# Optimization experiments

Hardware: AMD Instinct MI355X
Metric: run time of the kernel (lower is better)

The kernel has to match this reference:

```python
import jax, jax.numpy as jnp
import numpy as np

EPS = 1e-12

def _l2n(x):
    return x / jnp.sqrt(jnp.maximum(jnp.sum(x * x, axis=-1, keepdims=True), EPS))

def _sn_kernel(w, u):
    # One power iteration of spectral normalization (TF SpectralNormalization._compute_weights).
    wr = w.reshape(-1, w.shape[-1])           # [in, out] (1x1 conv kernel flattened)
    v = _l2n(u @ wr.T)                        # [1, in]
    u2 = _l2n(v @ wr)                         # [1, out]
    u2 = jax.lax.stop_gradient(u2)
    v = jax.lax.stop_gradient(v)
    sigma = (v @ wr) @ u2.T                   # [1, 1]
    return w / sigma[0, 0]

def setup_inputs() -> dict:
    key = jax.random.key(0)
    ks = jax.random.split(key, 14)
    B, H, W, C = 8, 64, 64, 256
    d = C // 8
    inp = {
        'x':  jax.random.normal(ks[0], (B, H, W, C), jnp.float32),
        'wf': jax.random.normal(ks[1], (C, d), jnp.float32) * 0.02,
        'bf': jax.random.normal(ks[2], (d,), jnp.float32) * 0.02,
        'uf': jax.random.normal(ks[3], (1, d), jnp.float32) * 0.02,
        'wg': jax.random.normal(ks[4], (C, d), jnp.float32) * 0.02,
        'bg': jax.random.normal(ks[5], (d,), jnp.float32) * 0.02,
        'ug': jax.random.normal(ks[6], (1, d), jnp.float32) * 0.02,
        'wh': jax.random.normal(ks[7], (C, d), jnp.float32) * 0.02,
        'bh': jax.random.normal(ks[8], (d,), jnp.float32) * 0.02,
        'uh': jax.random.normal(ks[9], (1, d), jnp.float32) * 0.02,
        'wv': jax.random.normal(ks[10], (d, C), jnp.float32) * 0.02,
        'bv': jax.random.normal(ks[11], (C,), jnp.float32) * 0.02,
        'uv': jax.random.normal(ks[12], (1, C), jnp.float32) * 0.02,
        'gamma': jax.random.normal(ks[13], (1,), jnp.float32) * 0.1,
    }
    return inp

def reference(x, wf, bf, uf, wg, bg, ug, wh, bh, uh, wv, bv, uv, gamma):
    B, H, W, C = x.shape
    N = H * W
    # spectrally-normalized 1x1 conv kernels
    kf = _sn_kernel(wf, uf)
    kg = _sn_kernel(wg, ug)
    kh = _sn_kernel(wh, uh)
    kv = _sn_kernel(wv, uv)
    # 1x1 convs == channel matmuls on flattened spatial dims
    xf = x.reshape(B, N, C)
    f = xf @ kf + bf            # [B, N, d]
    g = xf @ kg + bg            # [B, N, d]
    h = xf @ kh + bh            # [B, N, d]
    s = jnp.einsum('bnd,bmd->bnm', g, f)   # [B, N, N]
    beta = jax.nn.softmax(s, axis=-1)
    v = jnp.einsum('bnm,bmd->bnd', beta, h)  # [B, N, d]
    o = v @ kv + bv             # [B, N, C]
    out = gamma[0] * o.reshape(B, H, W, C) + x
    return out
```

## Files before the change

### kernel.cpp

```cpp
#include <hip/hip_runtime.h>
#include <math.h>

typedef __attribute__((ext_vector_type(8))) short bf16x8;
typedef __attribute__((ext_vector_type(4))) short bf16x4;
typedef __attribute__((ext_vector_type(4))) float f32x4;

#define LOG2E 1.4426950408889634f

#if __has_builtin(__builtin_amdgcn_exp2f)
#define EXP2(x) __builtin_amdgcn_exp2f(x)
#else
#define EXP2(x) exp2f(x)
#endif

static __device__ __forceinline__ short f2bf(float f) {
  unsigned u = __builtin_bit_cast(unsigned, f);
  u = u + 0x7FFFu + ((u >> 16) & 1u);
  return (short)(u >> 16);
}

struct SigArgs {
  const float* w[4];
  const float* u[4];
  int din[4];
  int dout[4];
};

__global__ __launch_bounds__(256) void sigma_kernel(SigArgs a, float* scales) {
  int b = blockIdx.x;
  const float* w = a.w[b];
  const float* u = a.u[b];
  int IN = a.din[b], OUT = a.dout[b];
  __shared__ float sv[256];
  __shared__ float red[256];
  int tid = threadIdx.x;

  float t = 0.f;
  if (tid < IN) {
    for (int j = 0; j < OUT; j++) t += u[j] * w[tid * OUT + j];
  }
  red[tid] = t * t;
  __syncthreads();
  for (int st = 128; st > 0; st >>= 1) {
    if (tid < st) red[tid] += red[tid + st];
    __syncthreads();
  }
  float nv = sqrtf(fmaxf(red[0], 1e-12f));
  sv[tid] = (tid < IN) ? t / nv : 0.f;
  __syncthreads();

  float s2 = 0.f;
  if (tid < OUT) {
    float sum = 0.f;
    for (int i = 0; i < IN; i++) sum += sv[i] * w[i * OUT + tid];
    s2 = sum * sum;
  }
  red[tid] = s2;
  __syncthreads();
  for (int st = 128; st > 0; st >>= 1) {
    if (tid < st) red[tid] += red[tid + st];
    __syncthreads();
  }
  if (tid == 0) {
    float sum2 = red[0];
    float sigma = sum2 / sqrtf(fmaxf(sum2, 1e-12f));
    scales[b] = 1.0f / sigma;
  }
}

__global__ __launch_bounds__(256) void prep_weights(
    const float* __restrict__ wf, const float* __restrict__ wg,
    const float* __restrict__ wh, const float* __restrict__ wv,
    const float* __restrict__ scales, short* __restrict__ Wt,
    short* __restrict__ Kvt) {
  int idx = blockIdx.x * 256 + threadIdx.x;
  if (idx < 96 * 256) {
    int c = idx >> 8, k = idx & 255;
    int sel = c >> 5, cc = c & 31;
    const float* w = (sel == 0) ? wf : ((sel == 1) ? wg : wh);
    float sc = scales[sel] * ((sel == 1) ? LOG2E : 1.0f);
    Wt[idx] = f2bf(w[k * 32 + cc] * sc);
  } else {
    int i2 = idx - 96 * 256;
    if (i2 < 256 * 32) {
      int c = i2 >> 5, k = i2 & 31;
      Kvt[i2] = f2bf(wv[k * 256 + c] * scales[3]);
    }
  }
}

__global__ __launch_bounds__(256) void proj_kernel(
    const float* __restrict__ x, const short* __restrict__ Wt,
    const float* __restrict__ bf_, const float* __restrict__ bg_,
    const float* __restrict__ bh_, short* __restrict__ fo,
    short* __restrict__ go, short* __restrict__ hto) {
  __shared__ __align__(16) short xs[64][264];
  __shared__ float hsh[64][33];
  int row0 = blockIdx.x * 64;
  int tid = threadIdx.x;
  int wave = tid >> 6;
  int lane = tid & 63;
  int quad = lane >> 4, l16 = lane & 15;
  int rbase = row0 + wave * 16;

  const float4* xb = (const float4*)(x + (size_t)row0 * 256);
#pragma unroll
  for (int i = 0; i < 16; i++) {
    int e4 = i * 256 + tid;
    float4 v = xb[e4];
    int e = e4 * 4;
    int r = e >> 8, c = e & 255;
    bf16x4 s4;
    s4[0] = f2bf(v.x); s4[1] = f2bf(v.y); s4[2] = f2bf(v.z); s4[3] = f2bf(v.w);
    *(bf16x4*)&xs[r][c] = s4;
  }
  __syncthreads();

  f32x4 acc[6];
#pragma unroll
  for (int t = 0; t < 6; t++) acc[t] = (f32x4){0.f, 0.f, 0.f, 0.f};

#pragma unroll
  for (int kc = 0; kc < 256; kc += 32) {
    bf16x8 af = *(const bf16x8*)&xs[wave * 16 + l16][kc + quad * 8];
#pragma unroll
    for (int t = 0; t < 6; t++) {
      bf16x8 bfr = *(const bf16x8*)(Wt + (t * 16 + l16) * 256 + kc + quad * 8);
      acc[t] = __builtin_amdgcn_mfma_f32_16x16x32_bf16(af, bfr, acc[t], 0, 0, 0);
    }
  }

  int b = row0 >> 12;
  int n0 = row0 & 4095;
#pragma unroll
  for (int t = 0; t < 4; t++) {
    int c = t * 16 + l16;
    int sel = c >> 5, cc = c & 31;
    float bb = sel ? (bg_[cc] * LOG2E) : bf_[cc];
    short* dst = sel ? go : fo;
#pragma unroll
    for (int r = 0; r < 4; r++) {
      int row = rbase + quad * 4 + r;
      dst[(size_t)row * 32 + cc] = f2bf(acc[t][r] + bb);
    }
  }
#pragma unroll
  for (int t = 4; t < 6; t++) {
    int cc = (t - 4) * 16 + l16;
    float bb = bh_[cc];
#pragma unroll
    for (int r = 0; r < 4; r++) {
      hsh[wave * 16 + quad * 4 + r][cc] = acc[t][r] + bb;
    }
  }
  __syncthreads();
  {
    int d = threadIdx.x >> 3, ng = threadIdx.x & 7;
    bf16x8 tmp;
#pragma unroll
    for (int i = 0; i < 8; i++) tmp[i] = f2bf(hsh[ng * 8 + i][d]);
    *(bf16x8*)(hto + (size_t)(b * 32 + d) * 4096 + n0 + ng * 8) = tmp;
  }
}

__global__ __launch_bounds__(256) void attn_kernel(
    const short* __restrict__ g_, const short* __restrict__ f_,
    const short* __restrict__ ht_, short* __restrict__ po,
    float* __restrict__ ls) {
  __shared__ __align__(16) short psh[4][4][16][72];
  int b = blockIdx.y;
  int z = blockIdx.z;
  int wave = threadIdx.x >> 6;
  int lane = threadIdx.x & 63;
  int quad = lane >> 4, l16 = lane & 15;
  int qbase = blockIdx.x * 256 + wave * 64;
  int kc0 = z * 1024;

  const short* fb = f_ + (size_t)b * 4096 * 32;
  const short* hb = ht_ + (size_t)b * 32 * 4096;

  bf16x8 ga[4];
#pragma unroll
  for (int grp = 0; grp < 4; grp++)
    ga[grp] = *(const bf16x8*)(g_ + (size_t)(b * 4096 + qbase + grp * 16 + l16) * 32 +
                               quad * 8);

  f32x4 oacc[4][2];
#pragma unroll
  for (int grp = 0; grp < 4; grp++)
#pragma unroll
    for (int dt = 0; dt < 2; dt++) oacc[grp][dt] = (f32x4){0.f, 0.f, 0.f, 0.f};
  float lsum[4] = {0.f, 0.f, 0.f, 0.f};

  bf16x8 fA[4], fB[4];
#pragma unroll
  for (int t = 0; t < 4; t++)
    fA[t] = *(const bf16x8*)(fb + (size_t)(kc0 + t * 16 + l16) * 32 + quad * 8);

  auto chunk = [&](int kc, bf16x8* FC, bf16x8* FN) {
    bf16x8 hfr[2][2];
#pragma unroll
    for (int half = 0; half < 2; half++)
#pragma unroll
      for (int dt = 0; dt < 2; dt++)
        hfr[half][dt] = *(const bf16x8*)(hb + (size_t)(dt * 16 + l16) * 4096 +
                                         kc + half * 32 + quad * 8);
    int kn = (kc + 64 < kc0 + 1024) ? kc + 64 : kc0;
#pragma unroll
    for (int t = 0; t < 4; t++)
      FN[t] = *(const bf16x8*)(fb + (size_t)(kn + t * 16 + l16) * 32 + quad * 8);

#pragma unroll
    for (int grp = 0; grp < 4; grp++) {
      f32x4 s[4];
#pragma unroll
      for (int t = 0; t < 4; t++)
        s[t] = __builtin_amdgcn_mfma_f32_16x16x32_bf16(
            FC[t], ga[grp], (f32x4){0.f, 0.f, 0.f, 0.f}, 0, 0, 0);

      unsigned long long pk[4];
#pragma unroll
      for (int t = 0; t < 4; t++) {
        float p0 = EXP2(s[t][0]);
        float p1 = EXP2(s[t][1]);
        float p2 = EXP2(s[t][2]);
        float p3 = EXP2(s[t][3]);
        lsum[grp] += (p0 + p1) + (p2 + p3);
        unsigned lo = __builtin_amdgcn_perm(__builtin_bit_cast(unsigned, p1),
                                            __builtin_bit_cast(unsigned, p0),
                                            0x07060302u);
        unsigned hi = __builtin_amdgcn_perm(__builtin_bit_cast(unsigned, p3),
                                            __builtin_bit_cast(unsigned, p2),
                                            0x07060302u);
        pk[t] = ((unsigned long long)hi << 32) | lo;
      }

      unsigned long long* prow64 = (unsigned long long*)&psh[wave][grp][l16][0];
      asm volatile("" ::: "memory");
#pragma unroll
      for (int t = 0; t < 4; t++) prow64[4 * t + quad] = pk[t];
      asm volatile("" ::: "memory");

#pragma unroll
      for (int half = 0; half < 2; half++) {
        bf16x8 pa = *(const bf16x8*)(&psh[wave][grp][l16][half * 32 + quad * 8]);
#pragma unroll
        for (int dt = 0; dt < 2; dt++)
          oacc[grp][dt] = __builtin_amdgcn_mfma_f32_16x16x32_bf16(
              hfr[half][dt], pa, oacc[grp][dt], 0, 0, 0);
      }
    }
  };

  for (int it = 0; it < 16; it += 2) {
    chunk(kc0 + it * 64, fA, fB);
    chunk(kc0 + it * 64 + 64, fB, fA);
  }

#pragma unroll
  for (int grp = 0; grp < 4; grp++) {
    lsum[grp] += __shfl_xor(lsum[grp], 16);
    lsum[grp] += __shfl_xor(lsum[grp], 32);
  }

#pragma unroll
  for (int grp = 0; grp < 4; grp++) {
    size_t row = (size_t)b * 4096 + qbase + grp * 16 + l16;
    short* pod = po + ((size_t)z * 32768 + row) * 32;
#pragma unroll
    for (int dt = 0; dt < 2; dt++) {
      unsigned w0 = (unsigned)(unsigned short)f2bf(oacc[grp][dt][0]) |
                    ((unsigned)(unsigned short)f2bf(oacc[grp][dt][1]) << 16);
      unsigned w1 = (unsigned)(unsigned short)f2bf(oacc[grp][dt][2]) |
                    ((unsigned)(unsigned short)f2bf(oacc[grp][dt][3]) << 16);
      unsigned* dst = (unsigned*)(pod + dt * 16 + quad * 4);
      dst[0] = w0;
      dst[1] = w1;
    }
  }
  if (lane < 16) {
#pragma unroll
    for (int grp = 0; grp < 4; grp++)
      ls[(size_t)z * 32768 + (size_t)b * 4096 + qbase + grp * 16 + lane] = lsum[grp];
  }
}

__global__ __launch_bounds__(256) void outproj_kernel(
    const short* __restrict__ po, const float* __restrict__ ls,
    const short* __restrict__ Kvt, const float* __restrict__ bv,
    const float* __restrict__ gamma, const float* __restrict__ x,
    float* __restrict__ out) {
  __shared__ __align__(16) float osh[4][16][260];
  int row0 = blockIdx.x * 64;
  int wave = threadIdx.x >> 6, lane = threadIdx.x & 63;
  int quad = lane >> 4, l16 = lane & 15;
  int rbase = row0 + wave * 16;
  size_t row = (size_t)rbase + l16;

  float vacc[8];
#pragma unroll
  for (int j = 0; j < 8; j++) vacc[j] = 0.f;
#pragma unroll
  for (int z = 0; z < 4; z++) {
    const unsigned* p =
        (const unsigned*)(po + ((size_t)z * 32768 + row) * 32 + quad * 8);
#pragma unroll
    for (int j = 0; j < 4; j++) {
      unsigned w = p[j];
      vacc[2 * j] += __builtin_bit_cast(float, w << 16);
      vacc[2 * j + 1] += __builtin_bit_cast(float, w & 0xFFFF0000u);
    }
  }
  float l = ls[row] + ls[32768 + row] + ls[65536 + row] + ls[98304 + row];
  float inv = 1.0f / l;
  bf16x8 va;
#pragma unroll
  for (int j = 0; j < 8; j++) va[j] = f2bf(vacc[j] * inv);

  float gm = gamma[0];

  f32x4 acc[16];
#pragma unroll
  for (int t = 0; t < 16; t++) {
    bf16x8 kf = *(const bf16x8*)(Kvt + (t * 16 + l16) * 32 + quad * 8);
    acc[t] = __builtin_amdgcn_mfma_f32_16x16x32_bf16(
        va, kf, (f32x4){0.f, 0.f, 0.f, 0.f}, 0, 0, 0);
  }
#pragma unroll
  for (int t = 0; t < 16; t++) {
    float bb = bv[t * 16 + l16];
#pragma unroll
    for (int r = 0; r < 4; r++) {
      osh[wave][quad * 4 + r][t * 16 + l16] = acc[t][r] + bb;
    }
  }
  asm volatile("" ::: "memory");
  {
    int r_l = lane >> 2, c_l = lane & 3;
    int orow = row0 + wave * 16 + r_l;
    const float* oshr = &osh[wave][r_l][0];
    const float4* xr = (const float4*)(x + (size_t)orow * 256);
    float4* outr = (float4*)(out + (size_t)orow * 256);
#pragma unroll
    for (int i = 0; i < 16; i++) {
      int c4 = c_l + i * 4;
      float4 o4 = *(const float4*)&oshr[c4 * 4];
      float4 xv = xr[c4];
      float4 ov;
      ov.x = gm * o4.x + xv.x;
      ov.y = gm * o4.y + xv.y;
      ov.z = gm * o4.z + xv.z;
      ov.w = gm * o4.w + xv.w;
      outr[c4] = ov;
    }
  }
}

extern "C" void kernel_launch(void* const* d_in, const int* in_sizes, int n_in,
                              void* d_out, int out_size, void* d_ws,
                              size_t ws_size, hipStream_t stream) {
  const float* x = (const float*)d_in[0];
  const float* wf = (const float*)d_in[1];
  const float* bf = (const float*)d_in[2];
  const float* uf = (const float*)d_in[3];
  const float* wg = (const float*)d_in[4];
  const float* bg = (const float*)d_in[5];
  const float* ug = (const float*)d_in[6];
  const float* wh = (const float*)d_in[7];
  const float* bh = (const float*)d_in[8];
  const float* uh = (const float*)d_in[9];
  const float* wv = (const float*)d_in[10];
  const float* bv = (const float*)d_in[11];
  const float* uv = (const float*)d_in[12];
  const float* gamma = (const float*)d_in[13];
  float* out = (float*)d_out;

  char* ws = (char*)d_ws;
  float* scales = (float*)ws;
  short* Wt = (short*)(ws + 1024);
  short* Kvt = (short*)(ws + 64 * 1024);
  short* fo = (short*)(ws + 2u * 1024 * 1024);
  short* go = (short*)(ws + 4u * 1024 * 1024);
  short* hto = (short*)(ws + 6u * 1024 * 1024);
  short* po = (short*)(ws + 10u * 1024 * 1024);
  float* lsp = (float*)(ws + 18u * 1024 * 1024);

  SigArgs sa;
  sa.w[0] = wf; sa.u[0] = uf; sa.din[0] = 256; sa.dout[0] = 32;
  sa.w[1] = wg; sa.u[1] = ug; sa.din[1] = 256; sa.dout[1] = 32;
  sa.w[2] = wh; sa.u[2] = uh; sa.din[2] = 256; sa.dout[2] = 32;
  sa.w[3] = wv; sa.u[3] = uv; sa.din[3] = 32;  sa.dout[3] = 256;

  sigma_kernel<<<4, 256, 0, stream>>>(sa, scales);
  prep_weights<<<128, 256, 0, stream>>>(wf, wg, wh, wv, scales, Wt, Kvt);
  proj_kernel<<<512, 256, 0, stream>>>(x, Wt, bf, bg, bh, fo, go, hto);
  attn_kernel<<<dim3(16, 8, 4), 256, 0, stream>>>(go, fo, hto, po, lsp);
  outproj_kernel<<<512, 256, 0, stream>>>(po, lsp, Kvt, bv, gamma, x, out);
}
```

Before: 184.7 us.

## Software-pipeline PV MFMA one group behind the QK exp stage

Restructures the attention inner loop so each group's P·V MFMAs run one step behind its score/exp stage, reading the previous group's P tile from LDS before the current group's P is written. The P store and reload for the same group are no longer back to back, which gives the LDS write latency time to resolve and lets MFMA work overlap with exp work. This needs double-buffered H fragments across chunks, a zero-initialized prologue (zeroed P slot 3 and H buffer) and an epilogue that drains the last group. The cost is extra registers for the second H buffer, which may reduce occupancy.

```diff
diff --git a/kernel.cpp b/kernel.cpp
--- a/kernel.cpp
+++ b/kernel.cpp
@@ -192,31 +192,42 @@
     for (int dt = 0; dt < 2; dt++) oacc[grp][dt] = (f32x4){0.f, 0.f, 0.f, 0.f};
   float lsum[4] = {0.f, 0.f, 0.f, 0.f};
 
+  {
+    unsigned long long* p3 = (unsigned long long*)&psh[wave][3][l16][0];
+#pragma unroll
+    for (int t = 0; t < 4; t++) p3[4 * t + quad] = 0ull;
+  }
+  bf16x8 hA[2][2], hB[2][2];
+#pragma unroll
+  for (int half = 0; half < 2; half++)
+#pragma unroll
+    for (int dt = 0; dt < 2; dt++) hB[half][dt] = (bf16x8){0,0,0,0,0,0,0,0};
+
   bf16x8 fA[4], fB[4];
 #pragma unroll
   for (int t = 0; t < 4; t++)
     fA[t] = *(const bf16x8*)(fb + (size_t)(kc0 + t * 16 + l16) * 32 + quad * 8);
 
-  auto chunk = [&](int kc, bf16x8* FC, bf16x8* FN) {
-    bf16x8 hfr[2][2];
+  auto chunk = [&](int kc, bf16x8* FC, bf16x8* FN, bf16x8 (*HC)[2],
+                   bf16x8 (*HP)[2]) {
 #pragma unroll
     for (int half = 0; half < 2; half++)
 #pragma unroll
       for (int dt = 0; dt < 2; dt++)
-        hfr[half][dt] = *(const bf16x8*)(hb + (size_t)(dt * 16 + l16) * 4096 +
-                                         kc + half * 32 + quad * 8);
+        HC[half][dt] = *(const bf16x8*)(hb + (size_t)(dt * 16 + l16) * 4096 +
+                                        kc + half * 32 + quad * 8);
     int kn = (kc + 64 < kc0 + 1024) ? kc + 64 : kc0;
 #pragma unroll
     for (int t = 0; t < 4; t++)
       FN[t] = *(const bf16x8*)(fb + (size_t)(kn + t * 16 + l16) * 32 + quad * 8);
 
 #pragma unroll
-    for (int grp = 0; grp < 4; grp++) {
+    for (int g = 0; g < 4; g++) {
       f32x4 s[4];
 #pragma unroll
       for (int t = 0; t < 4; t++)
         s[t] = __builtin_amdgcn_mfma_f32_16x16x32_bf16(
-            FC[t], ga[grp], (f32x4){0.f, 0.f, 0.f, 0.f}, 0, 0, 0);
+            FC[t], ga[g], (f32x4){0.f, 0.f, 0.f, 0.f}, 0, 0, 0);
 
       unsigned long long pk[4];
 #pragma unroll
@@ -225,7 +236,7 @@
         float p1 = EXP2(s[t][1]);
         float p2 = EXP2(s[t][2]);
         float p3 = EXP2(s[t][3]);
-        lsum[grp] += (p0 + p1) + (p2 + p3);
+        lsum[g] += (p0 + p1) + (p2 + p3);
         unsigned lo = __builtin_amdgcn_perm(__builtin_bit_cast(unsigned, p1),
                                             __builtin_bit_cast(unsigned, p0),
                                             0x07060302u);
@@ -235,26 +246,42 @@
         pk[t] = ((unsigned long long)hi << 32) | lo;
       }
 
-      unsigned long long* prow64 = (unsigned long long*)&psh[wave][grp][l16][0];
+      {
+        const int pg = (g == 0) ? 3 : (g - 1);
+        bf16x8(*H)[2] = (g == 0) ? HP : HC;
+        const short* base = &psh[wave][pg][l16][0];
+#pragma unroll
+        for (int half = 0; half < 2; half++) {
+          bf16x8 pa = *(const bf16x8*)(base + half * 32 + quad * 8);
+#pragma unroll
+          for (int dt = 0; dt < 2; dt++)
+            oacc[pg][dt] = __builtin_amdgcn_mfma_f32_16x16x32_bf16(
+                H[half][dt], pa, oacc[pg][dt], 0, 0, 0);
+        }
+      }
+
       asm volatile("" ::: "memory");
+      unsigned long long* prow64 = (unsigned long long*)&psh[wave][g][l16][0];
 #pragma unroll
       for (int t = 0; t < 4; t++) prow64[4 * t + quad] = pk[t];
       asm volatile("" ::: "memory");
-
-#pragma unroll
-      for (int half = 0; half < 2; half++) {
-        bf16x8 pa = *(const bf16x8*)(&psh[wave][grp][l16][half * 32 + quad * 8]);
-#pragma unroll
-        for (int dt = 0; dt < 2; dt++)
-          oacc[grp][dt] = __builtin_amdgcn_mfma_f32_16x16x32_bf16(
-              hfr[half][dt], pa, oacc[grp][dt], 0, 0, 0);
-      }
     }
   };
 
   for (int it = 0; it < 16; it += 2) {
-    chunk(kc0 + it * 64, fA, fB);
-    chunk(kc0 + it * 64 + 64, fB, fA);
+    chunk(kc0 + it * 64, fA, fB, hA, hB);
+    chunk(kc0 + it * 64 + 64, fB, fA, hB, hA);
+  }
+  {
+    const short* base = &psh[wave][3][l16][0];
+#pragma unroll
+    for (int half = 0; half < 2; half++) {
+      bf16x8 pa = *(const bf16x8*)(base + half * 32 + quad * 8);
+#pragma unroll
+      for (int dt = 0; dt < 2; dt++)
+        oacc[3][dt] = __builtin_amdgcn_mfma_f32_16x16x32_bf16(
+            hB[half][dt], pa, oacc[3][dt], 0, 0, 0);
+    }
   }
 
 #pragma unroll
```

Result: no change. 188.3 us (+1.9%).

## Split attention keys into eight chunks and drop F-fragment double buffering

Applied to the files above, without the earlier changes.

The key dimension is now split eight ways instead of four, so the attention kernel launches twice as many blocks, each covering 512 keys, and the output projection sums eight partial results. The attention kernel gains a launch bound of four blocks per CU, and the manual double-buffered F prefetch is replaced by a simple in-loop load to cut register pressure. The aim is more occupancy and parallelism in the attention kernel. The cost is double the partial-output traffic in the reduction and more exposed load latency now that prefetching is gone.

```diff
diff --git a/kernel.cpp b/kernel.cpp
--- a/kernel.cpp
+++ b/kernel.cpp
@@ -163,7 +163,7 @@
   }
 }
 
-__global__ __launch_bounds__(256) void attn_kernel(
+__global__ __launch_bounds__(256, 4) void attn_kernel(
     const short* __restrict__ g_, const short* __restrict__ f_,
     const short* __restrict__ ht_, short* __restrict__ po,
     float* __restrict__ ls) {
@@ -174,7 +174,7 @@
   int lane = threadIdx.x & 63;
   int quad = lane >> 4, l16 = lane & 15;
   int qbase = blockIdx.x * 256 + wave * 64;
-  int kc0 = z * 1024;
+  int kc0 = z * 512;
 
   const short* fb = f_ + (size_t)b * 4096 * 32;
   const short* hb = ht_ + (size_t)b * 32 * 4096;
@@ -192,69 +192,55 @@
     for (int dt = 0; dt < 2; dt++) oacc[grp][dt] = (f32x4){0.f, 0.f, 0.f, 0.f};
   float lsum[4] = {0.f, 0.f, 0.f, 0.f};
 
-  bf16x8 fA[4], fB[4];
-#pragma unroll
-  for (int t = 0; t < 4; t++)
-    fA[t] = *(const bf16x8*)(fb + (size_t)(kc0 + t * 16 + l16) * 32 + quad * 8);
-
-  auto chunk = [&](int kc, bf16x8* FC, bf16x8* FN) {
-    bf16x8 hfr[2][2];
+  for (int kc = kc0; kc < kc0 + 512; kc += 64) {
+    bf16x8 F[4];
+#pragma unroll
+    for (int t = 0; t < 4; t++)
+      F[t] = *(const bf16x8*)(fb + (size_t)(kc + t * 16 + l16) * 32 + quad * 8);
+    bf16x8 H[2][2];
 #pragma unroll
     for (int half = 0; half < 2; half++)
 #pragma unroll
       for (int dt = 0; dt < 2; dt++)
-        hfr[half][dt] = *(const bf16x8*)(hb + (size_t)(dt * 16 + l16) * 4096 +
-                                         kc + half * 32 + quad * 8);
-    int kn = (kc + 64 < kc0 + 1024) ? kc + 64 : kc0;
-#pragma unroll
-    for (int t = 0; t < 4; t++)
-      FN[t] = *(const bf16x8*)(fb + (size_t)(kn + t * 16 + l16) * 32 + quad * 8);
-
-#pragma unroll
-    for (int grp = 0; grp < 4; grp++) {
+        H[half][dt] = *(const bf16x8*)(hb + (size_t)(dt * 16 + l16) * 4096 +
+                                       kc + half * 32 + quad * 8);
+
+#pragma unroll
+    for (int g = 0; g < 4; g++) {
       f32x4 s[4];
 #pragma unroll
       for (int t = 0; t < 4; t++)
         s[t] = __builtin_amdgcn_mfma_f32_16x16x32_bf16(
-            FC[t], ga[grp], (f32x4){0.f, 0.f, 0.f, 0.f}, 0, 0, 0);
-
-      unsigned long long pk[4];
+            F[t], ga[g], (f32x4){0.f, 0.f, 0.f, 0.f}, 0, 0, 0);
+
+      unsigned long long* prow64 = (unsigned long long*)&psh[wave][g][l16][0];
 #pragma unroll
       for (int t = 0; t < 4; t++) {
         float p0 = EXP2(s[t][0]);
         float p1 = EXP2(s[t][1]);
         float p2 = EXP2(s[t][2]);
         float p3 = EXP2(s[t][3]);
-        lsum[grp] += (p0 + p1) + (p2 + p3);
+        lsum[g] += (p0 + p1) + (p2 + p3);
         unsigned lo = __builtin_amdgcn_perm(__builtin_bit_cast(unsigned, p1),
                                             __builtin_bit_cast(unsigned, p0),
                                             0x07060302u);
         unsigned hi = __builtin_amdgcn_perm(__builtin_bit_cast(unsigned, p3),
                                             __builtin_bit_cast(unsigned, p2),
                                             0x07060302u);
-        pk[t] = ((unsigned long long)hi << 32) | lo;
+        prow64[4 * t + quad] = ((unsigned long long)hi << 32) | lo;
       }
-
-      unsigned long long* prow64 = (unsigned long long*)&psh[wave][grp][l16][0];
       asm volatile("" ::: "memory");
-#pragma unroll
-      for (int t = 0; t < 4; t++) prow64[4 * t + quad] = pk[t];
+
+#pragma unroll
+      for (int half = 0; half < 2; half++) {
+        bf16x8 pa = *(const bf16x8*)(&psh[wave][g][l16][half * 32 + quad * 8]);
+#pragma unroll
+        for (int dt = 0; dt < 2; dt++)
+          oacc[g][dt] = __builtin_amdgcn_mfma_f32_16x16x32_bf16(
+              H[half][dt], pa, oacc[g][dt], 0, 0, 0);
+      }
       asm volatile("" ::: "memory");
-
-#pragma unroll
-      for (int half = 0; half < 2; half++) {
-        bf16x8 pa = *(const bf16x8*)(&psh[wave][grp][l16][half * 32 + quad * 8]);
-#pragma unroll
-        for (int dt = 0; dt < 2; dt++)
-          oacc[grp][dt] = __builtin_amdgcn_mfma_f32_16x16x32_bf16(
-              hfr[half][dt], pa, oacc[grp][dt], 0, 0, 0);
-      }
-    }
-  };
-
-  for (int it = 0; it < 16; it += 2) {
-    chunk(kc0 + it * 64, fA, fB);
-    chunk(kc0 + it * 64 + 64, fB, fA);
+    }
   }
 
 #pragma unroll
@@ -300,8 +286,9 @@
   float vacc[8];
 #pragma unroll
   for (int j = 0; j < 8; j++) vacc[j] = 0.f;
-#pragma unroll
-  for (int z = 0; z < 4; z++) {
+  float l = 0.f;
+#pragma unroll
+  for (int z = 0; z < 8; z++) {
     const unsigned* p =
         (const unsigned*)(po + ((size_t)z * 32768 + row) * 32 + quad * 8);
 #pragma unroll
@@ -310,8 +297,8 @@
       vacc[2 * j] += __builtin_bit_cast(float, w << 16);
       vacc[2 * j + 1] += __builtin_bit_cast(float, w & 0xFFFF0000u);
     }
-  }
-  float l = ls[row] + ls[32768 + row] + ls[65536 + row] + ls[98304 + row];
+    l += ls[(size_t)z * 32768 + row];
+  }
   float inv = 1.0f / l;
   bf16x8 va;
 #pragma unroll
@@ -383,7 +370,7 @@
   short* go = (short*)(ws + 4u * 1024 * 1024);
   short* hto = (short*)(ws + 6u * 1024 * 1024);
   short* po = (short*)(ws + 10u * 1024 * 1024);
-  float* lsp = (float*)(ws + 18u * 1024 * 1024);
+  float* lsp = (float*)(ws + 26u * 1024 * 1024);
 
   SigArgs sa;
   sa.w[0] = wf; sa.u[0] = uf; sa.din[0] = 256; sa.dout[0] = 32;
@@ -394,6 +381,6 @@
   sigma_kernel<<<4, 256, 0, stream>>>(sa, scales);
   prep_weights<<<128, 256, 0, stream>>>(wf, wg, wh, wv, scales, Wt, Kvt);
   proj_kernel<<<512, 256, 0, stream>>>(x, Wt, bf, bg, bh, fo, go, hto);
-  attn_kernel<<<dim3(16, 8, 4), 256, 0, stream>>>(go, fo, hto, po, lsp);
+  attn_kernel<<<dim3(16, 8, 8), 256, 0, stream>>>(go, fo, hto, po, lsp);
   outproj_kernel<<<512, 256, 0, stream>>>(po, lsp, Kvt, bv, gamma, x, out);
 }
```

Result: no change. 185.3 us (+0.3%).
